# Kernel tuning notes

Measured on AMD Instinct MI355X. Metric: run time of the kernel, lower is better.

The kernel has to match this reference:

```python
import jax, jax.numpy as jnp
import numpy as np

MAX_DIST = 8
GUIDANCE_WEIGHT = 0.4
EPS_MAG = 1e-6
EPS_COS = 1e-8
EPS_WSUM = 1e-8


def setup_inputs() -> dict:
    key = jax.random.key(0)
    k1, k2 = jax.random.split(key)
    embeddings = jax.random.normal(k1, (4, 2048, 1024), dtype=jnp.float32)
    guidance_trajectories = jax.random.normal(k2, (512, 1024), dtype=jnp.float32)
    return {"embeddings": embeddings, "guidance_trajectories": guidance_trajectories}


def reference(embeddings, guidance_trajectories):
    B, S, D = embeddings.shape
    W = min(MAX_DIST, S - 1)  # fixed max window size

    # consecutive-token trajectory vectors: diffs[t] = emb[t+1] - emb[t]
    diffs = embeddings[:, 1:, :] - embeddings[:, :-1, :]          # [B, S-1, D]

    # sliding windows of the last W diffs ending at pos-1
    pos = jnp.arange(S)[:, None]                                  # [S, 1]
    k = jnp.arange(W)[None, :]                                    # [1, W]
    idx = pos - W + k                                             # diff index per slot
    valid = (idx >= 0) & (pos >= 1)                               # [S, W]
    windows = diffs[:, jnp.clip(idx, 0, S - 2), :]                # [B, S, W, D]

    # torch.linspace(0.1, 1.0, w) weights, per-position window size w = min(pos, W);
    # valid entries occupy the last w slots of the W-wide window.
    w = jnp.minimum(pos, W)                                       # [S, 1]
    j = k - (W - w)                                               # local index within window
    lin = jnp.where(w > 1, 0.1 + 0.9 * j / jnp.maximum(w - 1, 1), 0.1)
    pos_weights = jnp.where(valid, lin, 0.0).astype(embeddings.dtype)  # [S, W]

    # normalize trajectory vectors, zero where magnitude <= 1e-6
    mag = jnp.linalg.norm(windows, axis=-1, keepdims=True)        # [B, S, W, 1]
    is_valid_mag = mag > EPS_MAG
    normed = jnp.where(is_valid_mag, windows / jnp.where(is_valid_mag, mag, 1.0), 0.0)

    mag_weights = jnp.tanh(mag * 2.0)                             # [B, S, W, 1]
    combined = pos_weights[None, :, :, None] * mag_weights        # [B, S, W, 1]

    # guidance influence: softmax over cosine similarity to guidance bank
    g_norm = jnp.linalg.norm(guidance_trajectories, axis=-1)      # [G]
    a_norm = jnp.linalg.norm(normed, axis=-1)                     # [B, S, W]
    dots = jnp.einsum('bswd,gd->bswg', normed, guidance_trajectories)
    sims = dots / (jnp.maximum(a_norm, EPS_COS)[..., None] * jnp.maximum(g_norm, EPS_COS))
    g_weights = jax.nn.softmax(sims * 2.0, axis=-1)               # [B, S, W, G]
    influence = jnp.einsum('bswg,gd->bswd', g_weights, guidance_trajectories)
    blended = (1.0 - GUIDANCE_WEIGHT) * normed + GUIDANCE_WEIGHT * influence

    weight_sum = jnp.maximum(combined.sum(axis=2), EPS_WSUM)      # [B, S, 1]
    trajectories = (blended * combined).sum(axis=2) / weight_sum  # [B, S, D]
    return trajectories
```

## Files before the change

### kernel.cpp

```cpp
#include <hip/hip_runtime.h>
#include <math.h>

#define B_ 4
#define S_ 2048
#define D_ 1024
#define G_ 512
#define T_ 2047
#define MTO 32
#define NR 48
#define ABST2 1032
#define VST 520

typedef __attribute__((ext_vector_type(8))) short short8;
typedef __attribute__((ext_vector_type(4))) short s16x4;
typedef __attribute__((ext_vector_type(4))) float f32x4;

#define WSOFF_RG2 0u
#define WSOFF_BP1 4096u
#define WSOFF_BP2 (4096u + 1048576u)

__device__ inline short to_bf16(float f) {
    union { float f; unsigned u; } v; v.f = f;
    unsigned r = v.u + 0x7fffu + ((v.u >> 16) & 1u);
    return (short)(r >> 16);
}
__device__ inline float fb(unsigned short h) {
    union { unsigned u; float f; } v;
    v.u = ((unsigned)h) << 16;
    return v.f;
}
__device__ inline float fbs(short h) { return fb((unsigned short)h); }
__device__ inline f32x4 MF(short8 a, short8 b, f32x4 c) {
    return __builtin_amdgcn_mfma_f32_16x16x32_bf16(a, b, c, 0, 0, 0);
}

#define RAWBAR() do {                                            \
    __builtin_amdgcn_sched_barrier(0);                           \
    asm volatile("s_waitcnt lgkmcnt(0)" ::: "memory");           \
    __builtin_amdgcn_s_barrier();                                \
    __builtin_amdgcn_sched_barrier(0);                           \
} while (0)

__global__ __launch_bounds__(256) void prep_kernel(const float* __restrict__ guid,
                                                   float* __restrict__ rg2,
                                                   short8* __restrict__ Bp1,
                                                   short8* __restrict__ Bp2) {
    int bid = blockIdx.x, tid = threadIdx.x;
    if (bid < 128) {
        int wave = tid >> 6, lane = tid & 63;
        int g = bid * 4 + wave;
        const float4* gp = (const float4*)(guid + (size_t)g * D_);
        float ss = 0.f;
#pragma unroll
        for (int i = 0; i < 4; ++i) {
            float4 v = gp[lane + 64 * i];
            ss += v.x * v.x + v.y * v.y + v.z * v.z + v.w * v.w;
        }
#pragma unroll
        for (int m = 32; m >= 1; m >>= 1) ss += __shfl_xor(ss, m, 64);
        if (lane == 0) rg2[g] = 2.0f / fmaxf(sqrtf(ss), 1e-8f);
#pragma unroll
        for (int h = 0; h < 2; ++h) {
            int kg = lane + 64 * h;
            const float* src = guid + (size_t)g * D_ + kg * 8;
            short8 v;
#pragma unroll
            for (int j = 0; j < 8; ++j) v[j] = to_bf16(src[j]);
            Bp1[(size_t)kg * G_ + g] = v;
        }
    } else {
        int gg = bid - 128;
#pragma unroll
        for (int dd = 0; dd < 4; ++dd) {
            int d = tid + 256 * dd;
            short8 v;
#pragma unroll
            for (int j = 0; j < 8; ++j) v[j] = to_bf16(guid[(size_t)(gg * 8 + j) * D_ + d]);
            Bp2[(size_t)gg * D_ + d] = v;
        }
    }
}

#define G1Q3(ksv, q)  {                                                           \
    short8 a0 = *(const short8*)&ABs[l15][(ksv) * 32 + quad * 8];                 \
    short8 a1 = *(const short8*)&ABs[16 + l15][(ksv) * 32 + quad * 8];            \
    short8 a2 = *(const short8*)&ABs[32 + l15][(ksv) * 32 + quad * 8];            \
    acc1[0][0] = MF(a0, q[0], acc1[0][0]); acc1[0][1] = MF(a0, q[1], acc1[0][1]); \
    acc1[1][0] = MF(a1, q[0], acc1[1][0]); acc1[1][1] = MF(a1, q[1], acc1[1][1]); \
    acc1[2][0] = MF(a2, q[0], acc1[2][0]); acc1[2][1] = MF(a2, q[1], acc1[2][1]); }

__global__ __launch_bounds__(1024, 4) void fused_kernel(const float* __restrict__ emb,
                                                        const short8* __restrict__ Bp1,
                                                        const short8* __restrict__ Bp2,
                                                        const float* __restrict__ rg2,
                                                        float* __restrict__ out) {
    __shared__ short ABs[NR][ABST2];
    __shared__ short Vs[MTO][VST];
    __shared__ float rg2s[G_];
    __shared__ float pred[NR][16];
    __shared__ float magS[NR], rmagS[NR], mrS[NR], cvS[NR];
    __shared__ float rwsS[MTO];

    const int tid = threadIdx.x;
    const int wave = tid >> 6, lane = tid & 63;
    const int l15 = lane & 15, quad = lane >> 4;
    const int bid = blockIdx.x;
    const int b = bid >> 6;
    const int s0 = (bid & 63) << 5;
    const bool edge = (s0 == 0);

    if (tid < G_) rg2s[tid] = rg2[tid];

#pragma unroll
    for (int ii = 0; ii < 3; ++ii) {
        int rr = wave + 16 * ii;
        int t = s0 - 8 + rr;
        bool valid = (t >= 0) && (rr < 39);
        float ss = 0.f;
        if (valid) {
            const float4* p = (const float4*)(emb + ((size_t)b * S_ + t) * D_);
#pragma unroll
            for (int j = 0; j < 4; ++j) {
                float4 x0 = p[lane + 64 * j];
                float4 x1 = p[lane + 64 * j + 256];
                float4 dv = make_float4(x1.x - x0.x, x1.y - x0.y, x1.z - x0.z, x1.w - x0.w);
                ss += dv.x * dv.x + dv.y * dv.y + dv.z * dv.z + dv.w * dv.w;
                s16x4 h;
                h[0] = to_bf16(dv.x); h[1] = to_bf16(dv.y);
                h[2] = to_bf16(dv.z); h[3] = to_bf16(dv.w);
                *(s16x4*)&ABs[rr][4 * lane + 256 * j] = h;
            }
        } else {
            s16x4 z = (s16x4)0;
#pragma unroll
            for (int j = 0; j < 4; ++j) *(s16x4*)&ABs[rr][4 * lane + 256 * j] = z;
        }
#pragma unroll
        for (int m = 32; m >= 1; m >>= 1) ss += __shfl_xor(ss, m, 64);
        float mag = sqrtf(ss);
        if (lane == 0) {
            magS[rr]  = tanhf(2.0f * mag);
            rmagS[rr] = (mag > 1e-6f) ? (1.0f / mag) : 0.0f;
        }
    }
    RAWBAR();

    if (tid < NR) mrS[tid] = 0.6f * magS[tid] * rmagS[tid];
    if (tid < MTO) {
        int w = edge ? ((tid < 8) ? tid : 8) : 8;
        float rw = (w > 1) ? 0.9f / (float)(w - 1) : 0.f;
        float s = 0.f;
#pragma unroll
        for (int a = 1; a <= 8; ++a) {
            float lin = (a <= w) ? ((w > 1) ? (0.1f + rw * (float)(w - a)) : 0.1f) : 0.f;
            s += lin * magS[tid + 8 - a];
        }
        rwsS[tid] = 1.0f / fmaxf(s, 1e-8f);
    }

    f32x4 acc1[3][2];
#pragma unroll
    for (int mt = 0; mt < 3; ++mt)
#pragma unroll
        for (int nt = 0; nt < 2; ++nt) acc1[mt][nt] = (f32x4)0.f;
    {
        const short8* Bb = Bp1 + (size_t)quad * G_ + wave * 32 + l15;
        short8 q0[2], q1[2], q2[2], q3[2];
        q0[0] = Bb[0];          q0[1] = Bb[16];
        q1[0] = Bb[4 * G_];     q1[1] = Bb[4 * G_ + 16];
        q2[0] = Bb[8 * G_];     q2[1] = Bb[8 * G_ + 16];
        q3[0] = Bb[12 * G_];    q3[1] = Bb[12 * G_ + 16];
#pragma unroll
        for (int k4 = 0; k4 < 32; k4 += 4) {
            G1Q3(k4 + 0, q0); if (k4 < 28) { q0[0] = Bb[(size_t)(k4 + 4) * 4 * G_]; q0[1] = Bb[(size_t)(k4 + 4) * 4 * G_ + 16]; }
            G1Q3(k4 + 1, q1); if (k4 < 28) { q1[0] = Bb[(size_t)(k4 + 5) * 4 * G_]; q1[1] = Bb[(size_t)(k4 + 5) * 4 * G_ + 16]; }
            G1Q3(k4 + 2, q2); if (k4 < 28) { q2[0] = Bb[(size_t)(k4 + 6) * 4 * G_]; q2[1] = Bb[(size_t)(k4 + 6) * 4 * G_ + 16]; }
            G1Q3(k4 + 3, q3); if (k4 < 28) { q3[0] = Bb[(size_t)(k4 + 7) * 4 * G_]; q3[1] = Bb[(size_t)(k4 + 7) * 4 * G_ + 16]; }
        }
    }
    RAWBAR();

    float np_[MTO];
    {
        float pr[8];
#pragma unroll
        for (int r = 0; r < 8; ++r) pr[r] = mrS[r] * fbs(ABs[r][tid]);
        if (!edge) {
#pragma unroll
            for (int i = 0; i < MTO; ++i) {
                float s = 0.f;
#pragma unroll
                for (int a = 1; a <= 8; ++a)
                    s += (0.1f + (0.9f / 7.f) * (float)(8 - a)) * pr[(i + 8 - a) & 7];
                np_[i] = s;
                if (i < 31) pr[i & 7] = mrS[i + 8] * fbs(ABs[i + 8][tid]);
            }
        } else {
#pragma unroll
            for (int i = 0; i < MTO; ++i) {
                int w = (i < 8) ? i : 8;
                float rw = (w > 1) ? 0.9f / (float)(w - 1) : 0.f;
                float s = 0.f;
#pragma unroll
                for (int a = 1; a <= 8; ++a) {
                    float lin = (a <= w) ? ((w > 1) ? (0.1f + rw * (float)(w - a)) : 0.1f) : 0.f;
                    s += lin * pr[(i + 8 - a) & 7];
                }
                np_[i] = s;
                if (i < 31) pr[i & 7] = mrS[i + 8] * fbs(ABs[i + 8][tid]);
            }
        }
    }

    float psum[3][4];
#pragma unroll
    for (int mt = 0; mt < 3; ++mt)
#pragma unroll
        for (int r2 = 0; r2 < 4; ++r2) psum[mt][r2] = 0.f;
    {
        float rmv[3][4];
#pragma unroll
        for (int mt = 0; mt < 3; ++mt)
#pragma unroll
            for (int r2 = 0; r2 < 4; ++r2) rmv[mt][r2] = rmagS[mt * 16 + quad * 4 + r2];
#pragma unroll
        for (int mt = 0; mt < 3; ++mt)
#pragma unroll
            for (int nt = 0; nt < 2; ++nt) {
                float rgv = rg2s[wave * 32 + nt * 16 + l15];
#pragma unroll
                for (int r2 = 0; r2 < 4; ++r2) {
                    float e = __expf(acc1[mt][nt][r2] * rgv * rmv[mt][r2]);
                    acc1[mt][nt][r2] = e;
                    psum[mt][r2] += e;
                }
            }
#pragma unroll
        for (int m = 8; m >= 1; m >>= 1)
#pragma unroll
            for (int mt = 0; mt < 3; ++mt)
#pragma unroll
                for (int r2 = 0; r2 < 4; ++r2)
                    psum[mt][r2] += __shfl_xor(psum[mt][r2], m, 16);
    }
    RAWBAR();
#pragma unroll
    for (int mt = 0; mt < 3; ++mt)
#pragma unroll
        for (int nt = 0; nt < 2; ++nt)
#pragma unroll
            for (int r2 = 0; r2 < 4; ++r2)
                ABs[mt * 16 + quad * 4 + r2][wave * 32 + nt * 16 + l15] =
                    to_bf16(acc1[mt][nt][r2]);
    if (l15 == 0) {
#pragma unroll
        for (int mt = 0; mt < 3; ++mt)
#pragma unroll
            for (int r2 = 0; r2 < 4; ++r2)
                pred[mt * 16 + quad * 4 + r2][wave] = psum[mt][r2];
    }
    RAWBAR();
    if (tid < NR) {
        float s = 0.f;
#pragma unroll
        for (int w2 = 0; w2 < 16; ++w2) s += pred[tid][w2];
        cvS[tid] = 0.4f * magS[tid] / s;
    }
    RAWBAR();

#pragma unroll
    for (int ii = 0; ii < 2; ++ii) {
        int i = wave * 2 + ii;
        int w = edge ? ((i < 8) ? i : 8) : 8;
        float rw = (w > 1) ? 0.9f / (float)(w - 1) : 0.f;
        float c[8];
#pragma unroll
        for (int a = 1; a <= 8; ++a) {
            float lin = (a <= w) ? ((w > 1) ? (0.1f + rw * (float)(w - a)) : 0.1f) : 0.f;
            c[a - 1] = lin * cvS[i + 8 - a];
        }
        float v[8];
#pragma unroll
        for (int j = 0; j < 8; ++j) v[j] = 0.f;
#pragma unroll
        for (int a = 1; a <= 8; ++a) {
            short8 e = *(const short8*)&ABs[i + 8 - a][lane * 8];
#pragma unroll
            for (int j = 0; j < 8; ++j) v[j] += c[a - 1] * fbs(e[j]);
        }
        short8 vo;
#pragma unroll
        for (int j = 0; j < 8; ++j) vo[j] = to_bf16(v[j]);
        *(short8*)&Vs[i][lane * 8] = vo;
    }
    RAWBAR();

    short* IPb = &ABs[0][0];
#pragma unroll
    for (int half = 0; half < 2; ++half) {
        f32x4 acc2[2][2];
#pragma unroll
        for (int mt = 0; mt < 2; ++mt)
#pragma unroll
            for (int nt = 0; nt < 2; ++nt) acc2[mt][nt] = (f32x4)0.f;
        const short8* Bb2 = Bp2 + (size_t)quad * D_ + wave * 64 + half * 32 + l15;
        short8 bc0 = Bb2[0], bc1 = Bb2[16], bn0, bn1;
#pragma unroll
        for (int ks = 0; ks < 16; ++ks) {
            if (ks < 15) {
                const short8* Bx = Bb2 + (size_t)(ks + 1) * 4 * D_;
                bn0 = Bx[0]; bn1 = Bx[16];
            }
            short8 a0 = *(const short8*)&Vs[l15][ks * 32 + quad * 8];
            short8 a1 = *(const short8*)&Vs[16 + l15][ks * 32 + quad * 8];
            acc2[0][0] = MF(a0, bc0, acc2[0][0]); acc2[0][1] = MF(a0, bc1, acc2[0][1]);
            acc2[1][0] = MF(a1, bc0, acc2[1][0]); acc2[1][1] = MF(a1, bc1, acc2[1][1]);
            bc0 = bn0; bc1 = bn1;
        }
#pragma unroll
        for (int mt = 0; mt < 2; ++mt)
#pragma unroll
            for (int ntl = 0; ntl < 2; ++ntl) {
                int d2 = wave * 64 + half * 32 + ntl * 16 + l15;
#pragma unroll
                for (int r2 = 0; r2 < 4; ++r2)
                    IPb[(size_t)(mt * 16 + quad * 4 + r2) * ABST2 + d2] =
                        to_bf16(acc2[mt][ntl][r2]);
            }
    }
    RAWBAR();

    {
        float* ob = out + ((size_t)b * S_ + s0) * D_ + tid;
#pragma unroll
        for (int i = 0; i < MTO; ++i) {
            float ip = fbs(IPb[(size_t)i * ABST2 + tid]);
            ob[(size_t)i * D_] = (np_[i] + ip) * rwsS[i];
        }
    }
}

extern "C" void kernel_launch(void* const* d_in, const int* in_sizes, int n_in,
                              void* d_out, int out_size, void* d_ws, size_t ws_size,
                              hipStream_t stream) {
    const float* emb  = (const float*)d_in[0];
    const float* guid = (const float*)d_in[1];
    float* out = (float*)d_out;
    char* ws = (char*)d_ws;

    float*  rg2 = (float*)(ws + WSOFF_RG2);
    short8* Bp1 = (short8*)(ws + WSOFF_BP1);
    short8* Bp2 = (short8*)(ws + WSOFF_BP2);

    prep_kernel<<<192, 256, 0, stream>>>(guid, rg2, Bp1, Bp2);
    fused_kernel<<<256, 1024, 0, stream>>>(emb, Bp1, Bp2, rg2, out);
}
```

Baseline: 121.1 us.

## Quantize similarity GEMM to int8 MFMA and restructure shared-memory staging

```diff
diff --git a/kernel.cpp b/kernel.cpp
--- a/kernel.cpp
+++ b/kernel.cpp
@@ -5,19 +5,22 @@
 #define S_ 2048
 #define D_ 1024
 #define G_ 512
-#define T_ 2047
 #define MTO 32
 #define NR 48
-#define ABST2 1032
+#define DHST 1032
+#define WST 520
+#define IPST 1032
+#define D8ST 1040
 #define VST 520
 
 typedef __attribute__((ext_vector_type(8))) short short8;
 typedef __attribute__((ext_vector_type(4))) short s16x4;
 typedef __attribute__((ext_vector_type(4))) float f32x4;
+typedef __attribute__((ext_vector_type(4))) int i32x4;
 
 #define WSOFF_RG2 0u
 #define WSOFF_BP1 4096u
-#define WSOFF_BP2 (4096u + 1048576u)
+#define WSOFF_BP2 528384u
 
 __device__ inline short to_bf16(float f) {
     union { float f; unsigned u; } v; v.f = f;
@@ -32,6 +35,15 @@
 __device__ inline float fbs(short h) { return fb((unsigned short)h); }
 __device__ inline f32x4 MF(short8 a, short8 b, f32x4 c) {
     return __builtin_amdgcn_mfma_f32_16x16x32_bf16(a, b, c, 0, 0, 0);
+}
+__device__ inline i32x4 MFI(i32x4 a, i32x4 b, i32x4 c) {
+    return __builtin_amdgcn_mfma_i32_16x16x64_i8(a, b, c, 0, 0, 0);
+}
+__device__ inline unsigned pk4(float x, float y, float z, float w, float qs) {
+    int a = (int)rintf(x * qs), b = (int)rintf(y * qs);
+    int c = (int)rintf(z * qs), d = (int)rintf(w * qs);
+    return (unsigned)(a & 255) | ((unsigned)(b & 255) << 8) |
+           ((unsigned)(c & 255) << 16) | ((unsigned)(d & 255) << 24);
 }
 
 #define RAWBAR() do {                                            \
@@ -42,32 +54,33 @@
 } while (0)
 
 __global__ __launch_bounds__(256) void prep_kernel(const float* __restrict__ guid,
-                                                   float* __restrict__ rg2,
-                                                   short8* __restrict__ Bp1,
+                                                   float* __restrict__ rg2q,
+                                                   i32x4* __restrict__ Bp1q,
                                                    short8* __restrict__ Bp2) {
     int bid = blockIdx.x, tid = threadIdx.x;
     if (bid < 128) {
         int wave = tid >> 6, lane = tid & 63;
         int g = bid * 4 + wave;
-        const float4* gp = (const float4*)(guid + (size_t)g * D_);
-        float ss = 0.f;
-#pragma unroll
-        for (int i = 0; i < 4; ++i) {
-            float4 v = gp[lane + 64 * i];
-            ss += v.x * v.x + v.y * v.y + v.z * v.z + v.w * v.w;
-        }
-#pragma unroll
-        for (int m = 32; m >= 1; m >>= 1) ss += __shfl_xor(ss, m, 64);
-        if (lane == 0) rg2[g] = 2.0f / fmaxf(sqrtf(ss), 1e-8f);
-#pragma unroll
-        for (int h = 0; h < 2; ++h) {
-            int kg = lane + 64 * h;
-            const float* src = guid + (size_t)g * D_ + kg * 8;
-            short8 v;
-#pragma unroll
-            for (int j = 0; j < 8; ++j) v[j] = to_bf16(src[j]);
-            Bp1[(size_t)kg * G_ + g] = v;
-        }
+        const float4* g4 = (const float4*)(guid + (size_t)g * D_);
+        float4 v[4]; float ss = 0.f, mx = 0.f;
+#pragma unroll
+        for (int c = 0; c < 4; ++c) {
+            float4 t = g4[lane * 4 + c]; v[c] = t;
+            ss += t.x * t.x + t.y * t.y + t.z * t.z + t.w * t.w;
+            mx = fmaxf(mx, fmaxf(fmaxf(fabsf(t.x), fabsf(t.y)),
+                                 fmaxf(fabsf(t.z), fabsf(t.w))));
+        }
+#pragma unroll
+        for (int m = 32; m >= 1; m >>= 1) {
+            ss += __shfl_xor(ss, m, 64);
+            mx = fmaxf(mx, __shfl_xor(mx, m, 64));
+        }
+        if (lane == 0) rg2q[g] = 2.f * (mx / 127.f) / fmaxf(sqrtf(ss), 1e-8f);
+        float qs = 127.f / fmaxf(mx, 1e-20f);
+        i32x4 o;
+#pragma unroll
+        for (int c = 0; c < 4; ++c) o[c] = (int)pk4(v[c].x, v[c].y, v[c].z, v[c].w, qs);
+        Bp1q[(size_t)lane * G_ + g] = o;
     } else {
         int gg = bid - 128;
 #pragma unroll
@@ -81,25 +94,32 @@
     }
 }
 
-#define G1Q3(ksv, q)  {                                                           \
-    short8 a0 = *(const short8*)&ABs[l15][(ksv) * 32 + quad * 8];                 \
-    short8 a1 = *(const short8*)&ABs[16 + l15][(ksv) * 32 + quad * 8];            \
-    short8 a2 = *(const short8*)&ABs[32 + l15][(ksv) * 32 + quad * 8];            \
-    acc1[0][0] = MF(a0, q[0], acc1[0][0]); acc1[0][1] = MF(a0, q[1], acc1[0][1]); \
-    acc1[1][0] = MF(a1, q[0], acc1[1][0]); acc1[1][1] = MF(a1, q[1], acc1[1][1]); \
-    acc1[2][0] = MF(a2, q[0], acc1[2][0]); acc1[2][1] = MF(a2, q[1], acc1[2][1]); }
+#define G1S(ksv, q)  {                                                            \
+    const char* abp = D8 + (ksv) * 64 + quad * 16;                                \
+    i32x4 a0 = *(const i32x4*)(abp + (size_t)l15 * D8ST);                         \
+    i32x4 a1 = *(const i32x4*)(abp + (size_t)(16 + l15) * D8ST);                  \
+    i32x4 a2 = *(const i32x4*)(abp + (size_t)(32 + l15) * D8ST);                  \
+    acc1[0][0] = MFI(a0, q[0], acc1[0][0]); acc1[0][1] = MFI(a0, q[1], acc1[0][1]); \
+    acc1[1][0] = MFI(a1, q[0], acc1[1][0]); acc1[1][1] = MFI(a1, q[1], acc1[1][1]); \
+    acc1[2][0] = MFI(a2, q[0], acc1[2][0]); acc1[2][1] = MFI(a2, q[1], acc1[2][1]); }
 
 __global__ __launch_bounds__(1024, 4) void fused_kernel(const float* __restrict__ emb,
-                                                        const short8* __restrict__ Bp1,
+                                                        const i32x4* __restrict__ Bp1q,
                                                         const short8* __restrict__ Bp2,
-                                                        const float* __restrict__ rg2,
+                                                        const float* __restrict__ rg2q,
                                                         float* __restrict__ out) {
-    __shared__ short ABs[NR][ABST2];
-    __shared__ short Vs[MTO][VST];
+    __shared__ __align__(16) char RA[80512];
+    __shared__ __align__(16) char RB[49920];
     __shared__ float rg2s[G_];
     __shared__ float pred[NR][16];
-    __shared__ float magS[NR], rmagS[NR], mrS[NR], cvS[NR];
+    __shared__ float magS[NR], rmvqS[NR], mrS[NR];
     __shared__ float rwsS[MTO];
+
+    short* DH = (short*)RA;
+    short* WD = (short*)RA;
+    short* IP = (short*)RA;
+    char*  D8 = RB;
+    short* V  = (short*)RB;
 
     const int tid = threadIdx.x;
     const int wave = tid >> 6, lane = tid & 63;
@@ -109,43 +129,76 @@
     const int s0 = (bid & 63) << 5;
     const bool edge = (s0 == 0);
 
-    if (tid < G_) rg2s[tid] = rg2[tid];
-
-#pragma unroll
-    for (int ii = 0; ii < 3; ++ii) {
-        int rr = wave + 16 * ii;
-        int t = s0 - 8 + rr;
-        bool valid = (t >= 0) && (rr < 39);
-        float ss = 0.f;
-        if (valid) {
-            const float4* p = (const float4*)(emb + ((size_t)b * S_ + t) * D_);
+    if (tid < G_) rg2s[tid] = rg2q[tid];
+
+    {
+        int w3 = wave * 3;
+        int tb = s0 - 8 + w3;
+        if (w3 < 39) {
+            const float* eb = emb + (size_t)b * S_ * D_;
+            float ssr[3] = {0.f, 0.f, 0.f}, mxr[3] = {0.f, 0.f, 0.f};
+            float4 dv0[4], dv1[4], dv2[4];
 #pragma unroll
             for (int j = 0; j < 4; ++j) {
-                float4 x0 = p[lane + 64 * j];
-                float4 x1 = p[lane + 64 * j + 256];
-                float4 dv = make_float4(x1.x - x0.x, x1.y - x0.y, x1.z - x0.z, x1.w - x0.w);
-                ss += dv.x * dv.x + dv.y * dv.y + dv.z * dv.z + dv.w * dv.w;
-                s16x4 h;
-                h[0] = to_bf16(dv.x); h[1] = to_bf16(dv.y);
-                h[2] = to_bf16(dv.z); h[3] = to_bf16(dv.w);
-                *(s16x4*)&ABs[rr][4 * lane + 256 * j] = h;
+                float4 x[4];
+#pragma unroll
+                for (int r = 0; r < 4; ++r) {
+                    int t = tb + r; t = t < 0 ? 0 : t;
+                    x[r] = ((const float4*)(eb + (size_t)t * D_))[lane + 64 * j];
+                }
+#pragma unroll
+                for (int i = 0; i < 3; ++i) {
+                    float4 d = make_float4(x[i + 1].x - x[i].x, x[i + 1].y - x[i].y,
+                                           x[i + 1].z - x[i].z, x[i + 1].w - x[i].w);
+                    ssr[i] += d.x * d.x + d.y * d.y + d.z * d.z + d.w * d.w;
+                    mxr[i] = fmaxf(mxr[i], fmaxf(fmaxf(fabsf(d.x), fabsf(d.y)),
+                                                 fmaxf(fabsf(d.z), fabsf(d.w))));
+                    if (i == 0) dv0[j] = d; else if (i == 1) dv1[j] = d; else dv2[j] = d;
+                }
+            }
+#pragma unroll
+            for (int i = 0; i < 3; ++i) {
+                int rr = w3 + i;
+                bool val = (tb + i >= 0) && (rr < 39);
+                float ss = ssr[i], mx = mxr[i];
+#pragma unroll
+                for (int m = 32; m >= 1; m >>= 1) {
+                    ss += __shfl_xor(ss, m, 64);
+                    mx = fmaxf(mx, __shfl_xor(mx, m, 64));
+                }
+                if (!val) { ss = 0.f; mx = 0.f; }
+                float mag = sqrtf(ss);
+                if (lane == 0) {
+                    bool ok = val && (mag > 1e-6f);
+                    float tw = tanhf(2.f * mag);
+                    magS[rr]  = val ? tw : 0.f;
+                    rmvqS[rr] = ok ? mx / (127.f * mag) : 0.f;
+                    mrS[rr]   = ok ? 0.6f * tw / mag : 0.f;
+                }
+                float qs = 127.f / fmaxf(mx, 1e-20f);
+#pragma unroll
+                for (int j = 0; j < 4; ++j) {
+                    float4 d = (i == 0) ? dv0[j] : (i == 1) ? dv1[j] : dv2[j];
+                    if (!val) d = make_float4(0.f, 0.f, 0.f, 0.f);
+                    s16x4 h;
+                    h[0] = to_bf16(d.x); h[1] = to_bf16(d.y);
+                    h[2] = to_bf16(d.z); h[3] = to_bf16(d.w);
+                    *(s16x4*)&DH[(size_t)rr * DHST + 4 * lane + 256 * j] = h;
+                    *(unsigned*)&D8[(size_t)rr * D8ST + 4 * lane + 256 * j] =
+                        val ? pk4(d.x, d.y, d.z, d.w, qs) : 0u;
+                }
             }
         } else {
-            s16x4 z = (s16x4)0;
-#pragma unroll
-            for (int j = 0; j < 4; ++j) *(s16x4*)&ABs[rr][4 * lane + 256 * j] = z;
-        }
-#pragma unroll
-        for (int m = 32; m >= 1; m >>= 1) ss += __shfl_xor(ss, m, 64);
-        float mag = sqrtf(ss);
-        if (lane == 0) {
-            magS[rr]  = tanhf(2.0f * mag);
-            rmagS[rr] = (mag > 1e-6f) ? (1.0f / mag) : 0.0f;
+#pragma unroll
+            for (int i = 0; i < 3; ++i) {
+                int rr = w3 + i;
+                *(i32x4*)&D8[(size_t)rr * D8ST + 16 * lane] = (i32x4)0;
+                if (lane == 0) { magS[rr] = 0.f; rmvqS[rr] = 0.f; mrS[rr] = 0.f; }
+            }
         }
     }
     RAWBAR();
 
-    if (tid < NR) mrS[tid] = 0.6f * magS[tid] * rmagS[tid];
     if (tid < MTO) {
         int w = edge ? ((tid < 8) ? tid : 8) : 8;
         float rw = (w > 1) ? 0.9f / (float)(w - 1) : 0.f;
@@ -158,33 +211,23 @@
         rwsS[tid] = 1.0f / fmaxf(s, 1e-8f);
     }
 
-    f32x4 acc1[3][2];
+    i32x4 acc1[3][2];
 #pragma unroll
     for (int mt = 0; mt < 3; ++mt)
 #pragma unroll
-        for (int nt = 0; nt < 2; ++nt) acc1[mt][nt] = (f32x4)0.f;
-    {
-        const short8* Bb = Bp1 + (size_t)quad * G_ + wave * 32 + l15;
-        short8 q0[2], q1[2], q2[2], q3[2];
-        q0[0] = Bb[0];          q0[1] = Bb[16];
-        q1[0] = Bb[4 * G_];     q1[1] = Bb[4 * G_ + 16];
-        q2[0] = Bb[8 * G_];     q2[1] = Bb[8 * G_ + 16];
-        q3[0] = Bb[12 * G_];    q3[1] = Bb[12 * G_ + 16];
-#pragma unroll
-        for (int k4 = 0; k4 < 32; k4 += 4) {
-            G1Q3(k4 + 0, q0); if (k4 < 28) { q0[0] = Bb[(size_t)(k4 + 4) * 4 * G_]; q0[1] = Bb[(size_t)(k4 + 4) * 4 * G_ + 16]; }
-            G1Q3(k4 + 1, q1); if (k4 < 28) { q1[0] = Bb[(size_t)(k4 + 5) * 4 * G_]; q1[1] = Bb[(size_t)(k4 + 5) * 4 * G_ + 16]; }
-            G1Q3(k4 + 2, q2); if (k4 < 28) { q2[0] = Bb[(size_t)(k4 + 6) * 4 * G_]; q2[1] = Bb[(size_t)(k4 + 6) * 4 * G_ + 16]; }
-            G1Q3(k4 + 3, q3); if (k4 < 28) { q3[0] = Bb[(size_t)(k4 + 7) * 4 * G_]; q3[1] = Bb[(size_t)(k4 + 7) * 4 * G_ + 16]; }
-        }
-    }
-    RAWBAR();
+        for (int nt = 0; nt < 2; ++nt) acc1[mt][nt] = (i32x4)0;
+    const i32x4* PB = Bp1q + (size_t)quad * G_ + wave * 32 + l15;
+    i32x4 q0[2], q1[2], q2[2], q3[2];
+    q0[0] = PB[0];        q0[1] = PB[16];
+    q1[0] = PB[2048];     q1[1] = PB[2048 + 16];
+    q2[0] = PB[4096];     q2[1] = PB[4096 + 16];
+    q3[0] = PB[6144];     q3[1] = PB[6144 + 16];
 
     float np_[MTO];
     {
         float pr[8];
 #pragma unroll
-        for (int r = 0; r < 8; ++r) pr[r] = mrS[r] * fbs(ABs[r][tid]);
+        for (int r = 0; r < 8; ++r) pr[r] = mrS[r] * fbs(DH[(size_t)r * DHST + tid]);
         if (!edge) {
 #pragma unroll
             for (int i = 0; i < MTO; ++i) {
@@ -193,7 +236,7 @@
                 for (int a = 1; a <= 8; ++a)
                     s += (0.1f + (0.9f / 7.f) * (float)(8 - a)) * pr[(i + 8 - a) & 7];
                 np_[i] = s;
-                if (i < 31) pr[i & 7] = mrS[i + 8] * fbs(ABs[i + 8][tid]);
+                if (i < 31) pr[i & 7] = mrS[i + 8] * fbs(DH[(size_t)(i + 8) * DHST + tid]);
             }
         } else {
 #pragma unroll
@@ -207,22 +250,37 @@
                     s += lin * pr[(i + 8 - a) & 7];
                 }
                 np_[i] = s;
-                if (i < 31) pr[i & 7] = mrS[i + 8] * fbs(ABs[i + 8][tid]);
-            }
-        }
-    }
-
+                if (i < 31) pr[i & 7] = mrS[i + 8] * fbs(DH[(size_t)(i + 8) * DHST + tid]);
+            }
+        }
+    }
+
+    {
+#pragma unroll
+        for (int k4 = 0; k4 < 16; k4 += 4) {
+            G1S(k4 + 0, q0); if (k4 < 12) { q0[0] = PB[(size_t)(k4 + 4) * 2048]; q0[1] = PB[(size_t)(k4 + 4) * 2048 + 16]; }
+            G1S(k4 + 1, q1); if (k4 < 12) { q1[0] = PB[(size_t)(k4 + 5) * 2048]; q1[1] = PB[(size_t)(k4 + 5) * 2048 + 16]; }
+            G1S(k4 + 2, q2); if (k4 < 12) { q2[0] = PB[(size_t)(k4 + 6) * 2048]; q2[1] = PB[(size_t)(k4 + 6) * 2048 + 16]; }
+            G1S(k4 + 3, q3); if (k4 < 12) { q3[0] = PB[(size_t)(k4 + 7) * 2048]; q3[1] = PB[(size_t)(k4 + 7) * 2048 + 16]; }
+        }
+    }
+
+    const short8* Bb2 = Bp2 + (size_t)quad * D_ + wave * 64 + l15;
+    short8 c0[4];
+#pragma unroll
+    for (int nt = 0; nt < 4; ++nt) c0[nt] = Bb2[nt * 16];
+
+    f32x4 ew[3][2];
     float psum[3][4];
-#pragma unroll
-    for (int mt = 0; mt < 3; ++mt)
-#pragma unroll
-        for (int r2 = 0; r2 < 4; ++r2) psum[mt][r2] = 0.f;
     {
         float rmv[3][4];
 #pragma unroll
         for (int mt = 0; mt < 3; ++mt)
 #pragma unroll
-            for (int r2 = 0; r2 < 4; ++r2) rmv[mt][r2] = rmagS[mt * 16 + quad * 4 + r2];
+            for (int r2 = 0; r2 < 4; ++r2) {
+                rmv[mt][r2] = rmvqS[mt * 16 + quad * 4 + r2];
+                psum[mt][r2] = 0.f;
+            }
 #pragma unroll
         for (int mt = 0; mt < 3; ++mt)
 #pragma unroll
@@ -230,8 +288,8 @@
                 float rgv = rg2s[wave * 32 + nt * 16 + l15];
 #pragma unroll
                 for (int r2 = 0; r2 < 4; ++r2) {
-                    float e = __expf(acc1[mt][nt][r2] * rgv * rmv[mt][r2]);
-                    acc1[mt][nt][r2] = e;
+                    float e = __expf((float)acc1[mt][nt][r2] * rgv * rmv[mt][r2]);
+                    ew[mt][nt][r2] = e;
                     psum[mt][r2] += e;
                 }
             }
@@ -244,14 +302,15 @@
                     psum[mt][r2] += __shfl_xor(psum[mt][r2], m, 16);
     }
     RAWBAR();
+
 #pragma unroll
     for (int mt = 0; mt < 3; ++mt)
 #pragma unroll
         for (int nt = 0; nt < 2; ++nt)
 #pragma unroll
             for (int r2 = 0; r2 < 4; ++r2)
-                ABs[mt * 16 + quad * 4 + r2][wave * 32 + nt * 16 + l15] =
-                    to_bf16(acc1[mt][nt][r2]);
+                WD[(size_t)(mt * 16 + quad * 4 + r2) * WST + wave * 32 + nt * 16 + l15] =
+                    to_bf16(ew[mt][nt][r2]);
     if (l15 == 0) {
 #pragma unroll
         for (int mt = 0; mt < 3; ++mt)
@@ -260,81 +319,102 @@
                 pred[mt * 16 + quad * 4 + r2][wave] = psum[mt][r2];
     }
     RAWBAR();
-    if (tid < NR) {
-        float s = 0.f;
-#pragma unroll
-        for (int w2 = 0; w2 < 16; ++w2) s += pred[tid][w2];
-        cvS[tid] = 0.4f * magS[tid] / s;
+
+    {
+        float sums[9];
+#pragma unroll
+        for (int r = 0; r < 9; ++r) {
+            int rr = 2 * wave + r;
+            float s = 0.f;
+#pragma unroll
+            for (int w2 = 0; w2 < 16; ++w2) s += pred[rr][w2];
+            sums[r] = s;
+        }
+#pragma unroll
+        for (int ii = 0; ii < 2; ++ii) {
+            int i = wave * 2 + ii;
+            int w = edge ? ((i < 8) ? i : 8) : 8;
+            float rw = (w > 1) ? 0.9f / (float)(w - 1) : 0.f;
+            float c[8];
+#pragma unroll
+            for (int a = 1; a <= 8; ++a) {
+                int rr = i + 8 - a;
+                float lin = (a <= w) ? ((w > 1) ? (0.1f + rw * (float)(w - a)) : 0.1f) : 0.f;
+                c[a - 1] = lin * 0.4f * magS[rr] / sums[rr - 2 * wave];
+            }
+            float v[8];
+#pragma unroll
+            for (int j = 0; j < 8; ++j) v[j] = 0.f;
+#pragma unroll
+            for (int a = 1; a <= 8; ++a) {
+                short8 e = *(const short8*)&WD[(size_t)(i + 8 - a) * WST + lane * 8];
+#pragma unroll
+                for (int j = 0; j < 8; ++j) v[j] += c[a - 1] * fbs(e[j]);
+            }
+            short8 vo;
+#pragma unroll
+            for (int j = 0; j < 8; ++j) vo[j] = to_bf16(v[j]);
+            *(short8*)&V[(size_t)i * VST + lane * 8] = vo;
+        }
     }
     RAWBAR();
 
-#pragma unroll
-    for (int ii = 0; ii < 2; ++ii) {
-        int i = wave * 2 + ii;
-        int w = edge ? ((i < 8) ? i : 8) : 8;
-        float rw = (w > 1) ? 0.9f / (float)(w - 1) : 0.f;
-        float c[8];
-#pragma unroll
-        for (int a = 1; a <= 8; ++a) {
-            float lin = (a <= w) ? ((w > 1) ? (0.1f + rw * (float)(w - a)) : 0.1f) : 0.f;
-            c[a - 1] = lin * cvS[i + 8 - a];
-        }
-        float v[8];
-#pragma unroll
-        for (int j = 0; j < 8; ++j) v[j] = 0.f;
-#pragma unroll
-        for (int a = 1; a <= 8; ++a) {
-            short8 e = *(const short8*)&ABs[i + 8 - a][lane * 8];
-#pragma unroll
-            for (int j = 0; j < 8; ++j) v[j] += c[a - 1] * fbs(e[j]);
-        }
-        short8 vo;
-#pragma unroll
-        for (int j = 0; j < 8; ++j) vo[j] = to_bf16(v[j]);
-        *(short8*)&Vs[i][lane * 8] = vo;
+    {
+        f32x4 acc2[2][4];
+#pragma unroll
+        for (int mt = 0; mt < 2; ++mt)
+#pragma unroll
+            for (int nt = 0; nt < 4; ++nt) acc2[mt][nt] = (f32x4)0.f;
+        short8 c1[4];
+#pragma unroll
+        for (int nt = 0; nt < 4; ++nt) c1[nt] = Bb2[(size_t)4 * D_ + nt * 16];
+#pragma unroll
+        for (int k2 = 0; k2 < 16; k2 += 2) {
+            {
+                short8 a0 = *(const short8*)&V[(size_t)l15 * VST + k2 * 32 + quad * 8];
+                short8 a1 = *(const short8*)&V[(size_t)(16 + l15) * VST + k2 * 32 + quad * 8];
+#pragma unroll
+                for (int nt = 0; nt < 4; ++nt) {
+                    acc2[0][nt] = MF(a0, c0[nt], acc2[0][nt]);
+                    acc2[1][nt] = MF(a1, c0[nt], acc2[1][nt]);
+                }
+                if (k2 < 14) {
+#pragma unroll
+                    for (int nt = 0; nt < 4; ++nt) c0[nt] = Bb2[(size_t)(k2 + 2) * 4 * D_ + nt * 16];
+                }
+            }
+            {
+                short8 a0 = *(const short8*)&V[(size_t)l15 * VST + (k2 + 1) * 32 + quad * 8];
+                short8 a1 = *(const short8*)&V[(size_t)(16 + l15) * VST + (k2 + 1) * 32 + quad * 8];
+#pragma unroll
+                for (int nt = 0; nt < 4; ++nt) {
+                    acc2[0][nt] = MF(a0, c1[nt], acc2[0][nt]);
+                    acc2[1][nt] = MF(a1, c1[nt], acc2[1][nt]);
+                }
+                if (k2 < 14) {
+#pragma unroll
+                    for (int nt = 0; nt < 4; ++nt) c1[nt] = Bb2[(size_t)(k2 + 3) * 4 * D_ + nt * 16];
+                }
+            }
+        }
+#pragma unroll
+        for (int mt = 0; mt < 2; ++mt)
+#pragma unroll
+            for (int nt = 0; nt < 4; ++nt) {
+                int d2 = wave * 64 + nt * 16 + l15;
+#pragma unroll
+                for (int r2 = 0; r2 < 4; ++r2)
+                    IP[(size_t)(mt * 16 + quad * 4 + r2) * IPST + d2] =
+                        to_bf16(acc2[mt][nt][r2]);
+            }
     }
     RAWBAR();
 
-    short* IPb = &ABs[0][0];
-#pragma unroll
-    for (int half = 0; half < 2; ++half) {
-        f32x4 acc2[2][2];
-#pragma unroll
-        for (int mt = 0; mt < 2; ++mt)
-#pragma unroll
-            for (int nt = 0; nt < 2; ++nt) acc2[mt][nt] = (f32x4)0.f;
-        const short8* Bb2 = Bp2 + (size_t)quad * D_ + wave * 64 + half * 32 + l15;
-        short8 bc0 = Bb2[0], bc1 = Bb2[16], bn0, bn1;
-#pragma unroll
-        for (int ks = 0; ks < 16; ++ks) {
-            if (ks < 15) {
-                const short8* Bx = Bb2 + (size_t)(ks + 1) * 4 * D_;
-                bn0 = Bx[0]; bn1 = Bx[16];
-            }
-            short8 a0 = *(const short8*)&Vs[l15][ks * 32 + quad * 8];
-            short8 a1 = *(const short8*)&Vs[16 + l15][ks * 32 + quad * 8];
-            acc2[0][0] = MF(a0, bc0, acc2[0][0]); acc2[0][1] = MF(a0, bc1, acc2[0][1]);
-            acc2[1][0] = MF(a1, bc0, acc2[1][0]); acc2[1][1] = MF(a1, bc1, acc2[1][1]);
-            bc0 = bn0; bc1 = bn1;
-        }
-#pragma unroll
-        for (int mt = 0; mt < 2; ++mt)
-#pragma unroll
-            for (int ntl = 0; ntl < 2; ++ntl) {
-                int d2 = wave * 64 + half * 32 + ntl * 16 + l15;
-#pragma unroll
-                for (int r2 = 0; r2 < 4; ++r2)
-                    IPb[(size_t)(mt * 16 + quad * 4 + r2) * ABST2 + d2] =
-                        to_bf16(acc2[mt][ntl][r2]);
-            }
-    }
-    RAWBAR();
-
     {
         float* ob = out + ((size_t)b * S_ + s0) * D_ + tid;
 #pragma unroll
         for (int i = 0; i < MTO; ++i) {
-            float ip = fbs(IPb[(size_t)i * ABST2 + tid]);
+            float ip = fbs(IP[(size_t)i * IPST + tid]);
             ob[(size_t)i * D_] = (np_[i] + ip) * rwsS[i];
         }
     }
@@ -348,10 +428,10 @@
     float* out = (float*)d_out;
     char* ws = (char*)d_ws;
 
-    float*  rg2 = (float*)(ws + WSOFF_RG2);
-    short8* Bp1 = (short8*)(ws + WSOFF_BP1);
+    float* rg2q = (float*)(ws + WSOFF_RG2);
+    i32x4* Bp1q = (i32x4*)(ws + WSOFF_BP1);
     short8* Bp2 = (short8*)(ws + WSOFF_BP2);
 
-    prep_kernel<<<192, 256, 0, stream>>>(guid, rg2, Bp1, Bp2);
-    fused_kernel<<<256, 1024, 0, stream>>>(emb, Bp1, Bp2, rg2, out);
-}
+    prep_kernel<<<192, 256, 0, stream>>>(guid, rg2q, Bp1q, Bp2);
+    fused_kernel<<<256, 1024, 0, stream>>>(emb, Bp1q, Bp2, rg2q, out);
+}
```

Measured after the change: 147.1 us. 1.22x slower.
